# Kernel tuning notes

Measured on AMD Instinct MI355X. Metric: run time of the kernel, lower is better.

The kernel has to match this reference:

```python
import jax, jax.numpy as jnp
import numpy as np

B, S, D, E, TOP_K = 4, 4096, 2048, 64, 2

def setup_inputs() -> dict:
    key = jax.random.key(0)
    k1, k2, k3, k4 = jax.random.split(key, 4)
    return {
        "mh_output": jax.random.normal(k1, (B, S, D), dtype=jnp.float32),
        "W_route": jax.random.normal(k2, (D, E), dtype=jnp.float32) * (1.0 / np.sqrt(D)),
        "b_route": jnp.zeros((E,), dtype=jnp.float32),
        "W_noise": jax.random.normal(k3, (D, E), dtype=jnp.float32) * (1.0 / np.sqrt(D)),
        "b_noise": jnp.zeros((E,), dtype=jnp.float32),
        "noise": jax.random.normal(k4, (B, S, E), dtype=jnp.float32),
    }

def reference(mh_output, W_route, b_route, W_noise, b_noise, noise):
    # logits / noise logits: [B, S, E]
    logits = jnp.einsum("bsd,de->bse", mh_output, W_route) + b_route
    noise_logits = jnp.einsum("bsd,de->bse", mh_output, W_noise) + b_noise
    noisy_logits = logits + noise * jax.nn.softplus(noise_logits)

    top_vals, indices = jax.lax.top_k(noisy_logits, TOP_K)  # [B,S,K]

    # scatter top-k values into a -inf-filled tensor, then softmax
    flat_vals = top_vals.reshape(-1, TOP_K)
    flat_idx = indices.reshape(-1, TOP_K)
    n_tok = flat_idx.shape[0]
    rows = jnp.arange(n_tok)[:, None]
    sparse = jnp.full((n_tok, E), -jnp.inf, dtype=noisy_logits.dtype)
    sparse = sparse.at[rows, flat_idx].set(flat_vals)
    probs = jax.nn.softmax(sparse, axis=-1).reshape(noisy_logits.shape)
    return probs, indices
```

## Files before the change

### kernel.cpp

```cpp
#include <hip/hip_runtime.h>
#include <math.h>

#define M_TOK 16384
#define D_DIM 2048
#define E_EXP 64
#define NCOL  128
#define BM    32
#define BK    64
#define NITER (D_DIM / BK)

#define ROW_STRIDE 144
#define PLANE (BM * ROW_STRIDE)
#define BUFSZ (3 * PLANE)
#define SMEM_BYTES (2 * BUFSZ)

typedef float         f32x4  __attribute__((ext_vector_type(4)));
typedef short         bf16x8 __attribute__((ext_vector_type(8)));
typedef unsigned int  uint;

#define MFMA_B16(a, b, c) __builtin_amdgcn_mfma_f32_16x16x32_bf16((a), (b), (c), 0, 0, 0)

__device__ __forceinline__ unsigned short bfrne(float f) {
    unsigned int u = __float_as_uint(f);
    return (unsigned short)((u + 0x7fffu + ((u >> 16) & 1u)) >> 16);
}
__device__ __forceinline__ float bfhi(unsigned short h) {
    return __uint_as_float((unsigned int)h << 16);
}

__device__ __forceinline__ bool beats(float va, int ia, float vb, int ib) {
    return (va > vb) || (va == vb && ia < ib);
}

__global__ __launch_bounds__(256) void prep_w(
    const float* __restrict__ Wr, const float* __restrict__ Wn,
    unsigned short* __restrict__ Wg)
{
    const int g    = blockIdx.x * 256 + threadIdx.x;
    const int lane = g & 63;
    const int cf   = (g >> 6) & 7;
    const int kblk = g >> 9;
    const int colL = (cf & 3) * 16 + (lane & 15);
    const float* __restrict__ W = (cf < 4) ? Wr : Wn;
    const int kbase = kblk * 32 + (lane >> 4) * 8;

    bf16x8 o0, o1, o2;
    #pragma unroll
    for (int j = 0; j < 8; ++j) {
        const float w = W[(size_t)(kbase + j) * E_EXP + colL];
        const unsigned short h0 = bfrne(w);
        const float r  = w - bfhi(h0);
        const unsigned short h1 = bfrne(r);
        const float r2 = r - bfhi(h1);
        const unsigned short h2 = bfrne(r2);
        o0[j] = (short)h0; o1[j] = (short)h1; o2[j] = (short)h2;
    }
    const size_t s0 = (((size_t)kblk * 3 + 0) * 8 + cf) * 64 + lane;
    const size_t s1 = (((size_t)kblk * 3 + 1) * 8 + cf) * 64 + lane;
    const size_t s2 = (((size_t)kblk * 3 + 2) * 8 + cf) * 64 + lane;
    *(bf16x8*)(Wg + s0 * 8) = o0;
    *(bf16x8*)(Wg + s1 * 8) = o1;
    *(bf16x8*)(Wg + s2 * 8) = o2;
}

__device__ __forceinline__ void load_b(const unsigned short* __restrict__ Wg,
                                       int it, int wc, int lane,
                                       bf16x8 (&Bv)[2][3])
{
    #pragma unroll
    for (int s = 0; s < 2; ++s) {
        const int kblk = it * 2 + s;
        #pragma unroll
        for (int p = 0; p < 3; ++p) {
            const size_t idx = (((size_t)kblk * 3 + p) * 8 + wc) * 64 + lane;
            Bv[s][p] = *(const bf16x8*)(Wg + idx * 8);
        }
    }
}

__device__ __forceinline__ void load_a(const float* __restrict__ A, int tokBase,
                                       int it, int tid, float4& x)
{
    const int row = tid >> 4;
    const int kc  = tid & 15;
    x = *(const float4*)(A + (size_t)(tokBase + row) * D_DIM + it * BK + kc * 4);
}

__device__ __forceinline__ void cvt_store(char* smem, int buf, int tid, const float4& x)
{
    const float v[4] = {x.x, x.y, x.z, x.w};
    uint t0[4], t1[4]; unsigned short h2[4];
    #pragma unroll
    for (int j = 0; j < 4; ++j) {
        const uint u = __float_as_uint(v[j]);
        t0[j] = u & 0xffff0000u;
        const float r = v[j] - __uint_as_float(t0[j]);
        const uint ru = __float_as_uint(r);
        t1[j] = ru & 0xffff0000u;
        const float r2 = r - __uint_as_float(t1[j]);
        h2[j] = bfrne(r2);
    }
    uint2 w0, w1, w2;
    w0.x = (t0[0] >> 16) | t0[1];  w0.y = (t0[2] >> 16) | t0[3];
    w1.x = (t1[0] >> 16) | t1[1];  w1.y = (t1[2] >> 16) | t1[3];
    w2.x = (uint)h2[0] | ((uint)h2[1] << 16);
    w2.y = (uint)h2[2] | ((uint)h2[3] << 16);

    const int row = tid >> 4;
    const int kc  = tid & 15;
    char* base = smem + buf * BUFSZ + row * ROW_STRIDE + kc * 8;
    *(uint2*)(base)             = w0;
    *(uint2*)(base + PLANE)     = w1;
    *(uint2*)(base + 2 * PLANE) = w2;
}

__device__ __forceinline__ void compute_iter(const char* Ab, int lane,
                                             const bf16x8 (&Bc)[2][3],
                                             f32x4 (&acch)[2], f32x4 (&accl)[2])
{
    #pragma unroll
    for (int s = 0; s < 2; ++s) {
        #pragma unroll
        for (int rf = 0; rf < 2; ++rf) {
            const int row = rf * 16 + (lane & 15);
            const int off = row * ROW_STRIDE + (s * 4 + (lane >> 4)) * 16;
            const bf16x8 a0 = *(const bf16x8*)(Ab + off);
            const bf16x8 a1 = *(const bf16x8*)(Ab + PLANE + off);
            const bf16x8 a2 = *(const bf16x8*)(Ab + 2 * PLANE + off);
            acch[rf] = MFMA_B16(a0, Bc[s][0], acch[rf]);
            accl[rf] = MFMA_B16(a0, Bc[s][1], accl[rf]);
            accl[rf] = MFMA_B16(a1, Bc[s][0], accl[rf]);
            accl[rf] = MFMA_B16(a1, Bc[s][1], accl[rf]);
            accl[rf] = MFMA_B16(a0, Bc[s][2], accl[rf]);
            accl[rf] = MFMA_B16(a2, Bc[s][0], accl[rf]);
        }
    }
}

#define LL_LD 132

__global__ __launch_bounds__(512) void fused_router(
    const float* __restrict__ A,
    const unsigned short* __restrict__ Wg,
    const float* __restrict__ br, const float* __restrict__ bn,
    const float* __restrict__ noise,
    float* __restrict__ probs, float* __restrict__ idxo)
{
    __shared__ __align__(16) char smem[SMEM_BYTES];

    const int tid  = threadIdx.x;
    const int lane = tid & 63;
    const int wc   = tid >> 6;
    const int tokBase = blockIdx.x * BM;

    f32x4 acch[2], accl[2];
    const f32x4 zero4 = {0.f, 0.f, 0.f, 0.f};
    acch[0] = zero4; acch[1] = zero4; accl[0] = zero4; accl[1] = zero4;

    bf16x8 B0[2][3], B1[2][3];
    float4 xE, xO;

    load_a(A, tokBase, 0, tid, xE);
    load_b(Wg, 0, wc, lane, B0);
    load_a(A, tokBase, 1, tid, xO);
    cvt_store(smem, 0, tid, xE);
    __syncthreads();

    #pragma unroll 1
    for (int it2 = 0; it2 < NITER / 2; ++it2) {
        const int ita = it2 * 2;
        const int itb = ita + 1;

        load_b(Wg, itb, wc, lane, B1);
        cvt_store(smem, 1, tid, xO);
        if (ita + 2 < NITER) load_a(A, tokBase, ita + 2, tid, xE);
        compute_iter(smem, lane, B0, acch, accl);
        __syncthreads();

        if (itb + 1 < NITER) load_b(Wg, itb + 1, wc, lane, B0);
        if (ita + 2 < NITER) cvt_store(smem, 0, tid, xE);
        if (itb + 2 < NITER) load_a(A, tokBase, itb + 2, tid, xO);
        compute_iter(smem + BUFSZ, lane, B1, acch, accl);
        __syncthreads();
    }

    float (*Llds)[LL_LD] = (float (*)[LL_LD])smem;
    {
        const int col = wc * 16 + (lane & 15);
        #pragma unroll
        for (int rf = 0; rf < 2; ++rf) {
            const int rowb = rf * 16 + (lane >> 4) * 4;
            #pragma unroll
            for (int r = 0; r < 4; ++r)
                Llds[rowb + r][col] = acch[rf][r] + accl[rf][r];
        }
    }
    __syncthreads();

    const int token = tid >> 4;
    const int s16   = tid & 15;
    const int tokG  = tokBase + token;

    float v0 = -INFINITY, v1 = -INFINITY;
    int i0 = 0, i1 = 0;
    {
        const float4 n4 = *(const float4*)(noise + (size_t)tokG * E_EXP + s16 * 4);
        const float4 b4 = *(const float4*)(br + s16 * 4);
        const float4 c4 = *(const float4*)(bn + s16 * 4);
        const float4 l4 = *(const float4*)(&Llds[token][s16 * 4]);
        const float4 m4 = *(const float4*)(&Llds[token][64 + s16 * 4]);
        const float nv[4] = {n4.x, n4.y, n4.z, n4.w};
        const float bv[4] = {b4.x, b4.y, b4.z, b4.w};
        const float cv[4] = {c4.x, c4.y, c4.z, c4.w};
        const float lv[4] = {l4.x, l4.y, l4.z, l4.w};
        const float mv[4] = {m4.x, m4.y, m4.z, m4.w};
        #pragma unroll
        for (int j = 0; j < 4; ++j) {
            const int e = s16 * 4 + j;
            const float lg = lv[j] + bv[j];
            const float nl = mv[j] + cv[j];
            const float sp = fmaxf(nl, 0.0f) + log1pf(expf(-fabsf(nl)));
            const float v  = fmaf(nv[j], sp, lg);
            if (beats(v, e, v0, i0))      { v1 = v0; i1 = i0; v0 = v; i0 = e; }
            else if (beats(v, e, v1, i1)) { v1 = v;  i1 = e; }
        }
    }
    #pragma unroll
    for (int m = 1; m < 16; m <<= 1) {
        const float w0 = __shfl_xor(v0, m), w1 = __shfl_xor(v1, m);
        const int   j0 = __shfl_xor(i0, m), j1 = __shfl_xor(i1, m);
        if (beats(v0, i0, w0, j0)) {
            if (!beats(v1, i1, w0, j0)) { v1 = w0; i1 = j0; }
        } else {
            if (beats(v0, i0, w1, j1)) { v1 = v0; i1 = i0; }
            else                       { v1 = w1; i1 = j1; }
            v0 = w0; i0 = j0;
        }
    }
    const float e1  = expf(v1 - v0);
    const float den = 1.0f + e1;
    const float p0 = 1.0f / den;
    const float p1 = e1 / den;

    float out[4];
    #pragma unroll
    for (int j = 0; j < 4; ++j) {
        const int e = s16 * 4 + j;
        out[j] = (e == i0) ? p0 : ((e == i1) ? p1 : 0.0f);
    }
    *(float4*)(probs + (size_t)tokG * E_EXP + s16 * 4) =
        make_float4(out[0], out[1], out[2], out[3]);
    if (s16 == 0)
        *(float2*)(idxo + (size_t)tokG * 2) = make_float2((float)i0, (float)i1);
}

extern "C" void kernel_launch(void* const* d_in, const int* in_sizes, int n_in,
                              void* d_out, int out_size, void* d_ws, size_t ws_size,
                              hipStream_t stream) {
    (void)in_sizes; (void)n_in; (void)out_size; (void)ws_size;
    const float* A  = (const float*)d_in[0];
    const float* Wr = (const float*)d_in[1];
    const float* br = (const float*)d_in[2];
    const float* Wn = (const float*)d_in[3];
    const float* bn = (const float*)d_in[4];
    const float* nz = (const float*)d_in[5];

    float* probs = (float*)d_out;
    float* idxo  = probs + (size_t)M_TOK * E_EXP;

    unsigned short* Wg = (unsigned short*)d_ws;

    prep_w<<<128, 256, 0, stream>>>(Wr, Wn, Wg);
    fused_router<<<M_TOK / BM, 512, 0, stream>>>(A, Wg, br, bn, nz, probs, idxo);
}
```

Baseline: 240.9 us.

## Use 32x32 MFMA with split-K across wave halves and fragment-major LDS layout

```diff
diff --git a/kernel.cpp b/kernel.cpp
--- a/kernel.cpp
+++ b/kernel.cpp
@@ -4,21 +4,18 @@
 #define M_TOK 16384
 #define D_DIM 2048
 #define E_EXP 64
-#define NCOL  128
 #define BM    32
-#define BK    64
-#define NITER (D_DIM / BK)
-
-#define ROW_STRIDE 144
-#define PLANE (BM * ROW_STRIDE)
-#define BUFSZ (3 * PLANE)
-#define SMEM_BYTES (2 * BUFSZ)
-
-typedef float         f32x4  __attribute__((ext_vector_type(4)));
+#define NT_H  16
+#define FRAG_B 1040
+#define TILE_B (12 * FRAG_B)
+#define SMEM_BYTES (4 * TILE_B)
+#define LL_LD 132
+
+typedef float         f32x16 __attribute__((ext_vector_type(16)));
 typedef short         bf16x8 __attribute__((ext_vector_type(8)));
 typedef unsigned int  uint;
 
-#define MFMA_B16(a, b, c) __builtin_amdgcn_mfma_f32_16x16x32_bf16((a), (b), (c), 0, 0, 0)
+#define MFMA32(a, b, c) __builtin_amdgcn_mfma_f32_32x32x16_bf16((a), (b), (c), 0, 0, 0)
 
 __device__ __forceinline__ unsigned short bfrne(float f) {
     unsigned int u = __float_as_uint(f);
@@ -36,13 +33,14 @@
     const float* __restrict__ Wr, const float* __restrict__ Wn,
     unsigned short* __restrict__ Wg)
 {
-    const int g    = blockIdx.x * 256 + threadIdx.x;
-    const int lane = g & 63;
-    const int cf   = (g >> 6) & 7;
-    const int kblk = g >> 9;
-    const int colL = (cf & 3) * 16 + (lane & 15);
-    const float* __restrict__ W = (cf < 4) ? Wr : Wn;
-    const int kbase = kblk * 32 + (lane >> 4) * 8;
+    const int g     = blockIdx.x * 256 + threadIdx.x;
+    const int lane  = g & 63;
+    const int ch    = (g >> 6) & 3;
+    const int kstep = g >> 8;
+    const int col   = ch * 32 + (lane & 31);
+    const float* __restrict__ W = (col < 64) ? Wr : Wn;
+    const int colL  = col & 63;
+    const int kbase = kstep * 16 + (lane >> 5) * 8;
 
     bf16x8 o0, o1, o2;
     #pragma unroll
@@ -55,38 +53,38 @@
         const unsigned short h2 = bfrne(r2);
         o0[j] = (short)h0; o1[j] = (short)h1; o2[j] = (short)h2;
     }
-    const size_t s0 = (((size_t)kblk * 3 + 0) * 8 + cf) * 64 + lane;
-    const size_t s1 = (((size_t)kblk * 3 + 1) * 8 + cf) * 64 + lane;
-    const size_t s2 = (((size_t)kblk * 3 + 2) * 8 + cf) * 64 + lane;
-    *(bf16x8*)(Wg + s0 * 8) = o0;
-    *(bf16x8*)(Wg + s1 * 8) = o1;
-    *(bf16x8*)(Wg + s2 * 8) = o2;
-}
-
-__device__ __forceinline__ void load_b(const unsigned short* __restrict__ Wg,
-                                       int it, int wc, int lane,
-                                       bf16x8 (&Bv)[2][3])
+    #pragma unroll
+    for (int p = 0; p < 3; ++p) {
+        const size_t idx = (((size_t)kstep * 3 + p) * 4 + ch) * 64 + lane;
+        const bf16x8 o = (p == 0) ? o0 : (p == 1) ? o1 : o2;
+        *(bf16x8*)(Wg + idx * 8) = o;
+    }
+}
+
+__device__ __forceinline__ void load_b_half(const unsigned short* __restrict__ Wg,
+                                            int t, int s0, int wc, int lane,
+                                            bf16x8 (&Bv)[2][3])
 {
     #pragma unroll
     for (int s = 0; s < 2; ++s) {
-        const int kblk = it * 2 + s;
+        const int kstep = t * 4 + s0 + s;
         #pragma unroll
         for (int p = 0; p < 3; ++p) {
-            const size_t idx = (((size_t)kblk * 3 + p) * 8 + wc) * 64 + lane;
-            Bv[s][p] = *(const bf16x8*)(Wg + idx * 8);
+            const size_t idx = (((size_t)kstep * 3 + p) * 4 + wc);
+            Bv[s][p] = *(const bf16x8*)(Wg + (idx << 9) + lane * 8);
         }
     }
 }
 
 __device__ __forceinline__ void load_a(const float* __restrict__ A, int tokBase,
-                                       int it, int tid, float4& x)
+                                       int t, int tid, float4& x)
 {
     const int row = tid >> 4;
     const int kc  = tid & 15;
-    x = *(const float4*)(A + (size_t)(tokBase + row) * D_DIM + it * BK + kc * 4);
-}
-
-__device__ __forceinline__ void cvt_store(char* smem, int buf, int tid, const float4& x)
+    x = *(const float4*)(A + (size_t)(tokBase + row) * D_DIM + t * 64 + kc * 4);
+}
+
+__device__ __forceinline__ void cvt_store(char* tbase, int tid, const float4& x)
 {
     const float v[4] = {x.x, x.y, x.z, x.w};
     uint t0[4], t1[4]; unsigned short h2[4];
@@ -106,38 +104,37 @@
     w2.x = (uint)h2[0] | ((uint)h2[1] << 16);
     w2.y = (uint)h2[2] | ((uint)h2[3] << 16);
 
-    const int row = tid >> 4;
-    const int kc  = tid & 15;
-    char* base = smem + buf * BUFSZ + row * ROW_STRIDE + kc * 8;
-    *(uint2*)(base)             = w0;
-    *(uint2*)(base + PLANE)     = w1;
-    *(uint2*)(base + 2 * PLANE) = w2;
-}
-
-__device__ __forceinline__ void compute_iter(const char* Ab, int lane,
-                                             const bf16x8 (&Bc)[2][3],
-                                             f32x4 (&acch)[2], f32x4 (&accl)[2])
-{
+    const int row   = tid >> 4;
+    const int kc    = tid & 15;
+    const int kstep = kc >> 2;
+    const int hoct  = (kc >> 1) & 1;
+    const int half  = kc & 1;
+    const int l     = hoct * 32 + row;
+    char* p = tbase + kstep * (3 * FRAG_B) + l * 16 + half * 8;
+    *(uint2*)(p)              = w0;
+    *(uint2*)(p + FRAG_B)     = w1;
+    *(uint2*)(p + 2 * FRAG_B) = w2;
+}
+
+__device__ __forceinline__ void compute_half(const char* tbase, int s0, int lane,
+                                             const bf16x8 (&Bv)[2][3],
+                                             f32x16& acch, f32x16& accl)
+{
+    const char* ap = tbase + lane * 16;
     #pragma unroll
     for (int s = 0; s < 2; ++s) {
-        #pragma unroll
-        for (int rf = 0; rf < 2; ++rf) {
-            const int row = rf * 16 + (lane & 15);
-            const int off = row * ROW_STRIDE + (s * 4 + (lane >> 4)) * 16;
-            const bf16x8 a0 = *(const bf16x8*)(Ab + off);
-            const bf16x8 a1 = *(const bf16x8*)(Ab + PLANE + off);
-            const bf16x8 a2 = *(const bf16x8*)(Ab + 2 * PLANE + off);
-            acch[rf] = MFMA_B16(a0, Bc[s][0], acch[rf]);
-            accl[rf] = MFMA_B16(a0, Bc[s][1], accl[rf]);
-            accl[rf] = MFMA_B16(a1, Bc[s][0], accl[rf]);
-            accl[rf] = MFMA_B16(a1, Bc[s][1], accl[rf]);
-            accl[rf] = MFMA_B16(a0, Bc[s][2], accl[rf]);
-            accl[rf] = MFMA_B16(a2, Bc[s][0], accl[rf]);
-        }
-    }
-}
-
-#define LL_LD 132
+        const int f = (s0 + s) * 3;
+        const bf16x8 a0 = *(const bf16x8*)(ap + (f + 0) * FRAG_B);
+        const bf16x8 a1 = *(const bf16x8*)(ap + (f + 1) * FRAG_B);
+        const bf16x8 a2 = *(const bf16x8*)(ap + (f + 2) * FRAG_B);
+        acch = MFMA32(a0, Bv[s][0], acch);
+        accl = MFMA32(a0, Bv[s][1], accl);
+        accl = MFMA32(a1, Bv[s][0], accl);
+        accl = MFMA32(a1, Bv[s][1], accl);
+        accl = MFMA32(a0, Bv[s][2], accl);
+        accl = MFMA32(a2, Bv[s][0], accl);
+    }
+}
 
 __global__ __launch_bounds__(512) void fused_router(
     const float* __restrict__ A,
@@ -150,49 +147,70 @@
 
     const int tid  = threadIdx.x;
     const int lane = tid & 63;
-    const int wc   = tid >> 6;
+    const int wid  = tid >> 6;
+    const int wc   = wid & 3;
+    const int kh   = wid >> 2;
     const int tokBase = blockIdx.x * BM;
 
-    f32x4 acch[2], accl[2];
-    const f32x4 zero4 = {0.f, 0.f, 0.f, 0.f};
-    acch[0] = zero4; acch[1] = zero4; accl[0] = zero4; accl[1] = zero4;
-
-    bf16x8 B0[2][3], B1[2][3];
-    float4 xE, xO;
-
-    load_a(A, tokBase, 0, tid, xE);
-    load_b(Wg, 0, wc, lane, B0);
-    load_a(A, tokBase, 1, tid, xO);
-    cvt_store(smem, 0, tid, xE);
+    f32x16 acch, accl;
+    #pragma unroll
+    for (int r = 0; r < 16; ++r) { acch[r] = 0.f; accl[r] = 0.f; }
+
+    char* st0a = smem;
+    char* st0b = smem + TILE_B;
+    char* st1a = smem + 2 * TILE_B;
+    char* st1b = smem + 3 * TILE_B;
+    const char* myBuf0 = smem + (kh * 2 + 0) * TILE_B;
+    const char* myBuf1 = smem + (kh * 2 + 1) * TILE_B;
+
+    float4 x0, x1, y0, y1;
+    bf16x8 Bv[2][3];
+
+    load_a(A, tokBase, 0,        tid, x0);
+    load_a(A, tokBase, NT_H,     tid, x1);
+    cvt_store(st0a, tid, x0);
+    cvt_store(st1a, tid, x1);
+    load_a(A, tokBase, 1,        tid, x0);
+    load_a(A, tokBase, NT_H + 1, tid, x1);
     __syncthreads();
 
     #pragma unroll 1
-    for (int it2 = 0; it2 < NITER / 2; ++it2) {
-        const int ita = it2 * 2;
-        const int itb = ita + 1;
-
-        load_b(Wg, itb, wc, lane, B1);
-        cvt_store(smem, 1, tid, xO);
-        if (ita + 2 < NITER) load_a(A, tokBase, ita + 2, tid, xE);
-        compute_iter(smem, lane, B0, acch, accl);
+    for (int it2 = 0; it2 < NT_H / 2; ++it2) {
+        const int itA = 2 * it2;
+        const int tA  = kh * NT_H + itA;
+
+        load_b_half(Wg, tA, 0, wc, lane, Bv);
+        cvt_store(st0b, tid, x0);
+        cvt_store(st1b, tid, x1);
+        if (itA + 2 < NT_H) {
+            load_a(A, tokBase, itA + 2,        tid, y0);
+            load_a(A, tokBase, NT_H + itA + 2, tid, y1);
+        }
+        compute_half(myBuf0, 0, lane, Bv, acch, accl);
+        load_b_half(Wg, tA, 2, wc, lane, Bv);
+        compute_half(myBuf0, 2, lane, Bv, acch, accl);
         __syncthreads();
 
-        if (itb + 1 < NITER) load_b(Wg, itb + 1, wc, lane, B0);
-        if (ita + 2 < NITER) cvt_store(smem, 0, tid, xE);
-        if (itb + 2 < NITER) load_a(A, tokBase, itb + 2, tid, xO);
-        compute_iter(smem + BUFSZ, lane, B1, acch, accl);
+        load_b_half(Wg, tA + 1, 0, wc, lane, Bv);
+        if (itA + 2 < NT_H) { cvt_store(st0a, tid, y0); cvt_store(st1a, tid, y1); }
+        if (itA + 3 < NT_H) {
+            load_a(A, tokBase, itA + 3,        tid, x0);
+            load_a(A, tokBase, NT_H + itA + 3, tid, x1);
+        }
+        compute_half(myBuf1, 0, lane, Bv, acch, accl);
+        load_b_half(Wg, tA + 1, 2, wc, lane, Bv);
+        compute_half(myBuf1, 2, lane, Bv, acch, accl);
         __syncthreads();
     }
 
-    float (*Llds)[LL_LD] = (float (*)[LL_LD])smem;
+    float (*Ll)[BM][LL_LD] = (float (*)[BM][LL_LD])smem;
     {
-        const int col = wc * 16 + (lane & 15);
+        const int col   = wc * 32 + (lane & 31);
+        const int rbase = 4 * (lane >> 5);
         #pragma unroll
-        for (int rf = 0; rf < 2; ++rf) {
-            const int rowb = rf * 16 + (lane >> 4) * 4;
-            #pragma unroll
-            for (int r = 0; r < 4; ++r)
-                Llds[rowb + r][col] = acch[rf][r] + accl[rf][r];
+        for (int r = 0; r < 16; ++r) {
+            const int row = (r & 3) + 8 * (r >> 2) + rbase;
+            Ll[kh][row][col] = acch[r] + accl[r];
         }
     }
     __syncthreads();
@@ -207,13 +225,15 @@
         const float4 n4 = *(const float4*)(noise + (size_t)tokG * E_EXP + s16 * 4);
         const float4 b4 = *(const float4*)(br + s16 * 4);
         const float4 c4 = *(const float4*)(bn + s16 * 4);
-        const float4 l4 = *(const float4*)(&Llds[token][s16 * 4]);
-        const float4 m4 = *(const float4*)(&Llds[token][64 + s16 * 4]);
+        const float4 la = *(const float4*)(&Ll[0][token][s16 * 4]);
+        const float4 lb = *(const float4*)(&Ll[1][token][s16 * 4]);
+        const float4 ma = *(const float4*)(&Ll[0][token][64 + s16 * 4]);
+        const float4 mb = *(const float4*)(&Ll[1][token][64 + s16 * 4]);
         const float nv[4] = {n4.x, n4.y, n4.z, n4.w};
         const float bv[4] = {b4.x, b4.y, b4.z, b4.w};
         const float cv[4] = {c4.x, c4.y, c4.z, c4.w};
-        const float lv[4] = {l4.x, l4.y, l4.z, l4.w};
-        const float mv[4] = {m4.x, m4.y, m4.z, m4.w};
+        const float lv[4] = {la.x + lb.x, la.y + lb.y, la.z + lb.z, la.w + lb.w};
+        const float mv[4] = {ma.x + mb.x, ma.y + mb.y, ma.z + mb.z, ma.w + mb.w};
         #pragma unroll
         for (int j = 0; j < 4; ++j) {
             const int e = s16 * 4 + j;
```

Result: faster. 230.3 us (-4.4%).
